# Kernel tuning notes

Hardware: AMD Instinct MI355X
Metric: run time of the kernel (lower is better)

Reference implementation:

```python
import jax, jax.numpy as jnp
import numpy as np

N = 1024   # nodes
E = 65536  # edges per relation
H = 2      # attention heads
NEG_SLOPE = 0.2


def _add_self_loops(ei, n):
    loop = jnp.arange(n, dtype=ei.dtype)
    return jnp.concatenate([ei, jnp.stack([loop, loop])], axis=1)


def _gat(x, ei, W, a_src, a_dst, bias, n):
    # PyG GATConv (heads=H, concat=True): project, edge attention, segment softmax, scatter-sum
    h, c = a_src.shape
    xp = (x @ W).reshape(n, h, c)                      # [n, H, C]
    src, dst = ei[0], ei[1]
    al_s = jnp.einsum('nhc,hc->nh', xp, a_src)         # [n, H]
    al_d = jnp.einsum('nhc,hc->nh', xp, a_dst)
    alpha = jax.nn.leaky_relu(al_s[src] + al_d[dst], NEG_SLOPE)  # [E, H]
    m = jax.ops.segment_max(alpha, dst, num_segments=n)
    m = jnp.where(jnp.isfinite(m), m, 0.0)
    m = jax.lax.stop_gradient(m)
    e = jnp.exp(alpha - m[dst])
    s = jax.ops.segment_sum(e, dst, num_segments=n)
    a = e / (s[dst] + 1e-16)                           # segment softmax over incoming edges
    out = jax.ops.segment_sum(xp[src] * a[:, :, None], dst, num_segments=n)
    return out.reshape(n, h * c) + bias


def setup_inputs():
    key = jax.random.key(0)
    ks = jax.random.split(key, 32)
    d = {}
    d['x'] = jax.random.normal(ks[0], (N, 256), dtype=jnp.float32)
    d['ei0'] = jax.random.randint(ks[1], (2, E), 0, N)
    d['ei1'] = jax.random.randint(ks[2], (2, E), 0, N)
    k = 3
    # layer 1: in 256 -> H*256 = 512 per relation
    for r in range(2):
        d[f'W1_{r}'] = jax.random.normal(ks[k], (256, H * 256), jnp.float32) * 0.0625; k += 1
        d[f'as1_{r}'] = jax.random.normal(ks[k], (H, 256), jnp.float32) * 0.0625; k += 1
        d[f'ad1_{r}'] = jax.random.normal(ks[k], (H, 256), jnp.float32) * 0.0625; k += 1
        d[f'b1_{r}'] = jnp.zeros((H * 256,), jnp.float32)
    # layer 2: in 512 -> H*64 = 128 per relation
    for r in range(2):
        d[f'W2_{r}'] = jax.random.normal(ks[k], (512, H * 64), jnp.float32) * 0.0442; k += 1
        d[f'as2_{r}'] = jax.random.normal(ks[k], (H, 64), jnp.float32) * 0.125; k += 1
        d[f'ad2_{r}'] = jax.random.normal(ks[k], (H, 64), jnp.float32) * 0.125; k += 1
        d[f'b2_{r}'] = jnp.zeros((H * 64,), jnp.float32)
    d['w_lin'] = jax.random.normal(ks[k], (H * 64, 1), jnp.float32) * 0.088; k += 1
    d['b_lin'] = jnp.zeros((1,), jnp.float32)
    return d


def reference(x, ei0, ei1, W1_0, as1_0, ad1_0, b1_0, W1_1, as1_1, ad1_1, b1_1,
              W2_0, as2_0, ad2_0, b2_0, W2_1, as2_1, ad2_1, b2_1, w_lin, b_lin):
    e0 = _add_self_loops(ei0, N)
    e1 = _add_self_loops(ei1, N)
    # HeteroConv aggr='sum' over the two relations
    h1 = _gat(x, e0, W1_0, as1_0, ad1_0, b1_0, N) + _gat(x, e1, W1_1, as1_1, ad1_1, b1_1, N)
    h1 = jax.nn.relu(h1)
    h2 = _gat(h1, e0, W2_0, as2_0, ad2_0, b2_0, N) + _gat(h1, e1, W2_1, as2_1, ad2_1, b2_1, N)
    # dense pairwise sum over all node pairs: [N*N, 128]
    pairs = (h2[:, None, :] + h2[None, :, :]).reshape(N * N, h2.shape[-1])
    return pairs @ w_lin + b_lin
```

## Files before the change

kernel.cpp:

```cpp
#include <hip/hip_runtime.h>
#include <hip/hip_bf16.h>


#define NEG_SLOPE 0.2f
static __device__ __forceinline__ float lrelu(float x){ return x > 0.f ? x : NEG_SLOPE * x; }

#define NN 1024
#define SLOTS 192

static __device__ __forceinline__ int norm_cnt(int raw){
    return raw < -1000000000 ? raw - (int)0xAAAAAAAAu : raw;
}

struct P {
    const float *x; const int *ei0, *ei1;
    const float *W1_0,*as1_0,*ad1_0,*b1_0, *W1_1,*as1_1,*ad1_1,*b1_1;
    const float *W2_0,*as2_0,*ad2_0,*b2_0, *W2_1,*as2_1,*ad2_1,*b2_1;
    const float *wlin, *blin;
    float *out;
    __hip_bfloat162 *xp1_0,*xp1_1;
    float *L1;
    float *wc;
    float *nb;
    float *q, *qb;
    int *cnt;
    unsigned short *eb;
    int E;
};

__global__ __launch_bounds__(256)
void k1_scatter_gemm1(P p){
    __shared__ float As[32][68];
    __shared__ float Bs[32][68];
    const int b = blockIdx.x, t = threadIdx.x;

    if (b < 128){
        const int TOT = p.E + NN;
        for (int i = b*256 + t; i < 2*TOT; i += 128*256){
            int r = i >= TOT, e = i - r*TOT;
            const int* ei = r ? p.ei1 : p.ei0;
            int src, dst;
            if (e < p.E){ src = ei[e]; dst = ei[p.E + e]; } else { src = dst = e - p.E; }
            int pos = norm_cnt(atomicAdd(&p.cnt[r*NN + dst], 1));
            if (pos >= 0 && pos < SLOTS)
                p.eb[(dst*2 + r)*SLOTS + pos] = (unsigned short)src;
        }
        return;
    }
    if (b >= 384){
        int idx2 = b - 384;
        int r = idx2 >> 2, k0 = (idx2 & 3) * 128;
        const float* W2 = r ? p.W2_1 : p.W2_0;
        const float* as2 = r ? p.as2_1 : p.as2_0;
        const float* ad2 = r ? p.ad2_1 : p.ad2_0;
        if (t < 128){
            int k = k0 + t;
            float sa[2] = {0.f,0.f}, da[2] = {0.f,0.f}, za[2] = {0.f,0.f};
            #pragma unroll
            for (int h = 0; h < 2; h++){
                for (int c = 0; c < 64; c++){
                    float w = W2[k*128 + h*64 + c];
                    sa[h] += w * as2[h*64 + c];
                    da[h] += w * ad2[h*64 + c];
                    za[h] += w * p.wlin[h*64 + c];
                }
            }
            float* wcr = p.wc + r*6*512;
            wcr[0*512 + k] = sa[0]; wcr[1*512 + k] = sa[1];
            wcr[2*512 + k] = da[0]; wcr[3*512 + k] = da[1];
            wcr[4*512 + k] = za[0]; wcr[5*512 + k] = za[1];
        }
        if (b == 384 && t == 128){
            float s = 0.f;
            for (int k = 0; k < 128; k++) s += (p.b2_0[k] + p.b2_1[k]) * p.wlin[k];
            p.qb[0] = s;
        }
        return;
    }
    int idx = b - 128;
    int r = idx >> 7, t2 = idx & 127;
    int m0 = (t2 >> 3) * 64, n0 = (t2 & 7) * 64;
    const float* B = r ? p.W1_1 : p.W1_0;
    __hip_bfloat162* C = r ? p.xp1_1 : p.xp1_0;
    int tx = t & 15, ty = t >> 4;
    const int am0 = t >> 3,  ac40 = t & 7;
    const int am1 = (256+t) >> 3, ac41 = t & 7;
    const int bk0 = t >> 4,  bc40 = t & 15;
    const int bk1 = (256+t) >> 4, bc41 = t & 15;
    float acc[4][4] = {};
    float4 a4[2], b4[2];
    a4[0] = *(const float4*)(p.x + (size_t)(m0+am0)*256 + 0 + ac40*4);
    a4[1] = *(const float4*)(p.x + (size_t)(m0+am1)*256 + 0 + ac41*4);
    b4[0] = *(const float4*)(B + (size_t)(0+bk0)*512 + n0 + bc40*4);
    b4[1] = *(const float4*)(B + (size_t)(0+bk1)*512 + n0 + bc41*4);
    for (int k0 = 0; k0 < 256; k0 += 32){
        __syncthreads();
        As[ac40*4+0][am0] = a4[0].x; As[ac40*4+1][am0] = a4[0].y;
        As[ac40*4+2][am0] = a4[0].z; As[ac40*4+3][am0] = a4[0].w;
        As[ac41*4+0][am1] = a4[1].x; As[ac41*4+1][am1] = a4[1].y;
        As[ac41*4+2][am1] = a4[1].z; As[ac41*4+3][am1] = a4[1].w;
        *(float4*)&Bs[bk0][bc40*4] = b4[0];
        *(float4*)&Bs[bk1][bc41*4] = b4[1];
        __syncthreads();
        if (k0 + 32 < 256){
            int kn = k0 + 32;
            a4[0] = *(const float4*)(p.x + (size_t)(m0+am0)*256 + kn + ac40*4);
            a4[1] = *(const float4*)(p.x + (size_t)(m0+am1)*256 + kn + ac41*4);
            b4[0] = *(const float4*)(B + (size_t)(kn+bk0)*512 + n0 + bc40*4);
            b4[1] = *(const float4*)(B + (size_t)(kn+bk1)*512 + n0 + bc41*4);
        }
        #pragma unroll
        for (int kk = 0; kk < 32; kk++){
            float4 av = *(const float4*)&As[kk][ty*4];
            float4 bv = *(const float4*)&Bs[kk][tx*4];
            float ar[4] = {av.x, av.y, av.z, av.w};
            float br[4] = {bv.x, bv.y, bv.z, bv.w};
            #pragma unroll
            for (int i = 0; i < 4; i++)
                #pragma unroll
                for (int j = 0; j < 4; j++)
                    acc[i][j] += ar[i] * br[j];
        }
    }
    #pragma unroll
    for (int i = 0; i < 4; i++){
        int row = m0 + ty*4 + i, col = n0 + tx*4;
        __hip_bfloat162 t0, t1;
        t0.x = __float2bfloat16(acc[i][0]); t0.y = __float2bfloat16(acc[i][1]);
        t1.x = __float2bfloat16(acc[i][2]); t1.y = __float2bfloat16(acc[i][3]);
        size_t o2 = ((size_t)row*512 + col) >> 1;
        C[o2] = t0; C[o2 + 1] = t1;
    }
    {
        int h = n0 >> 8;
        const float* as_ = r ? p.as1_1 : p.as1_0;
        const float* ad_ = r ? p.ad1_1 : p.ad1_0;
        float a_s[4], a_d[4];
        #pragma unroll
        for (int u = 0; u < 4; u++){
            a_s[u] = as_[n0 + tx*4 + u];
            a_d[u] = ad_[n0 + tx*4 + u];
        }
        #pragma unroll
        for (int i = 0; i < 4; i++){
            float ps = acc[i][0]*a_s[0] + acc[i][1]*a_s[1]
                     + acc[i][2]*a_s[2] + acc[i][3]*a_s[3];
            float pd = acc[i][0]*a_d[0] + acc[i][1]*a_d[1]
                     + acc[i][2]*a_d[2] + acc[i][3]*a_d[3];
            #pragma unroll
            for (int o = 8; o > 0; o >>= 1){
                ps += __shfl_down(ps, o, 16);
                pd += __shfl_down(pd, o, 16);
            }
            if (tx == 0){
                int row = m0 + ty*4 + i;
                atomicAdd(&p.L1[row*8 + r*4 + h],     ps);
                atomicAdd(&p.L1[row*8 + r*4 + 2 + h], pd);
            }
        }
    }
}

__global__ __launch_bounds__(256)
void k2_agg1(P p){
    __shared__ float wa0[256], wa1[256];
    __shared__ int ssrc[256];
    __shared__ float rr0[4], rr1[4], invs[2];
    __shared__ float pacc[4][64][8];
    const int v = blockIdx.x, t = threadIdx.x;
    const int par = t >> 6;
    const int c16 = t & 63;
    const bool head0 = c16 < 32;
    float acc[8] = {};
    #pragma unroll
    for (int r = 0; r < 2; r++){
        const __hip_bfloat162* xp = r ? p.xp1_1 : p.xp1_0;
        const unsigned short* eb = p.eb + (v*2 + r)*SLOTS;
        int end = min(norm_cnt(p.cnt[r*NN + v]), SLOTS);
        float ad0 = p.L1[v*8 + r*4 + 2], ad1 = p.L1[v*8 + r*4 + 3];
        float s0 = 0.f, s1 = 0.f;
        if (t < end){
            int s = eb[t];
            s0 = __expf(lrelu(p.L1[s*8 + r*4 + 0] + ad0));
            s1 = __expf(lrelu(p.L1[s*8 + r*4 + 1] + ad1));
            ssrc[t] = s * 256;
            wa0[t] = s0;
            wa1[t] = s1;
        }
        #pragma unroll
        for (int o = 32; o > 0; o >>= 1){
            s0 += __shfl_down(s0, o, 64);
            s1 += __shfl_down(s1, o, 64);
        }
        if ((t & 63) == 0){ rr0[t>>6] = s0; rr1[t>>6] = s1; }
        __syncthreads();
        if (t == 0){
            float S0 = 0.f, S1 = 0.f;
            #pragma unroll
            for (int i = 0; i < 4; i++){ S0 += rr0[i]; S1 += rr1[i]; }
            invs[0] = 1.f / (S0 + 1e-16f);
            invs[1] = 1.f / (S1 + 1e-16f);
        }
        __syncthreads();
        const float inv = head0 ? invs[0] : invs[1];
        #pragma unroll 4
        for (int i = par; i < end; i += 4){
            const __hip_bfloat162* rp = xp + ssrc[i] + c16*4;
            float4 raw = *(const float4*)rp;
            const __hip_bfloat162* w = (const __hip_bfloat162*)&raw;
            float a = (head0 ? wa0[i] : wa1[i]) * inv;
            #pragma unroll
            for (int u = 0; u < 4; u++){
                acc[2*u+0] += __bfloat162float(w[u].x) * a;
                acc[2*u+1] += __bfloat162float(w[u].y) * a;
            }
        }
        __syncthreads();
    }
    #pragma unroll
    for (int u = 0; u < 8; u++) pacc[par][c16][u] = acc[u];
    __syncthreads();
    if (par == 0){
        int cb = c16 * 8;
        float o[8];
        #pragma unroll
        for (int u = 0; u < 8; u++){
            float s = acc[u] + pacc[1][c16][u] + pacc[2][c16][u] + pacc[3][c16][u];
            s += p.b1_0[cb+u] + p.b1_1[cb+u];
            o[u] = s > 0.f ? s : 0.f;
        }
        const int slot[6] = {0, 1, 4, 5, 2, 3};
        #pragma unroll
        for (int r2 = 0; r2 < 2; r2++){
            #pragma unroll
            for (int j = 0; j < 6; j++){
                const float* w = p.wc + ((r2*6 + j) << 9) + cb;
                float s = o[0]*w[0] + o[1]*w[1] + o[2]*w[2] + o[3]*w[3]
                        + o[4]*w[4] + o[5]*w[5] + o[6]*w[6] + o[7]*w[7];
                #pragma unroll
                for (int off = 32; off > 0; off >>= 1) s += __shfl_down(s, off, 64);
                if (c16 == 0) p.nb[(v*2 + r2)*8 + slot[j]] = s;
            }
        }
    }
}

__global__ __launch_bounds__(256)
void k3_agg2(P p){
    __shared__ float red[2][2][4];
    const int b = blockIdx.x, t = threadIdx.x, lane = t & 63, wave = t >> 6;
    const int nl = wave >> 1, r = wave & 1;
    const int v = b*2 + nl;
    const unsigned short* eb = p.eb + (v*2 + r)*SLOTS;
    int end = min(norm_cnt(p.cnt[r*NN + v]), SLOTS);
    const float* nbv = p.nb + (v*2 + r)*8;
    float ld0 = nbv[4], ld1 = nbv[5];
    float d0 = 0.f, d1 = 0.f, n0 = 0.f, n1 = 0.f;
    for (int e = lane; e < end; e += 64){
        int s = eb[e];
        float4 g = *(const float4*)(p.nb + (s*2 + r)*8);
        float e0 = __expf(lrelu(g.x + ld0));
        float e1 = __expf(lrelu(g.y + ld1));
        d0 += e0; d1 += e1;
        n0 += e0 * g.z; n1 += e1 * g.w;
    }
    #pragma unroll
    for (int o = 1; o < 64; o <<= 1){
        d0 += __shfl_xor(d0, o, 64); d1 += __shfl_xor(d1, o, 64);
        n0 += __shfl_xor(n0, o, 64); n1 += __shfl_xor(n1, o, 64);
    }
    if (lane == 0){
        red[nl][r][0] = d0; red[nl][r][1] = d1;
        red[nl][r][2] = n0; red[nl][r][3] = n1;
    }
    __syncthreads();
    if (t == nl*128){
        float qv = p.qb[0];
        #pragma unroll
        for (int rr = 0; rr < 2; rr++){
            qv += red[nl][rr][2] / (red[nl][rr][0] + 1e-16f);
            qv += red[nl][rr][3] / (red[nl][rr][1] + 1e-16f);
        }
        p.q[v] = qv;
    }
}

__global__ __launch_bounds__(256)
void k4_pairs(P p){
    int i = blockIdx.x, t = threadIdx.x;
    float qi = p.q[i] + p.blin[0];
    float4 qj = ((const float4*)p.q)[t];
    float4 o = { qi + qj.x, qi + qj.y, qi + qj.z, qi + qj.w };
    ((float4*)p.out)[(size_t)i * 256 + t] = o;
}

extern "C" void kernel_launch(void* const* d_in, const int* in_sizes, int n_in,
                              void* d_out, int out_size, void* d_ws, size_t ws_size,
                              hipStream_t stream){
    P prm;
    prm.x    = (const float*)d_in[0];
    prm.ei0  = (const int*)d_in[1];
    prm.ei1  = (const int*)d_in[2];
    prm.W1_0 = (const float*)d_in[3];  prm.as1_0 = (const float*)d_in[4];
    prm.ad1_0 = (const float*)d_in[5]; prm.b1_0  = (const float*)d_in[6];
    prm.W1_1 = (const float*)d_in[7];  prm.as1_1 = (const float*)d_in[8];
    prm.ad1_1 = (const float*)d_in[9]; prm.b1_1  = (const float*)d_in[10];
    prm.W2_0 = (const float*)d_in[11]; prm.as2_0 = (const float*)d_in[12];
    prm.ad2_0 = (const float*)d_in[13]; prm.b2_0 = (const float*)d_in[14];
    prm.W2_1 = (const float*)d_in[15]; prm.as2_1 = (const float*)d_in[16];
    prm.ad2_1 = (const float*)d_in[17]; prm.b2_1 = (const float*)d_in[18];
    prm.wlin = (const float*)d_in[19];
    prm.blin = (const float*)d_in[20];
    prm.out  = (float*)d_out;
    prm.E    = in_sizes[1] / 2;
    const int N = NN;

    char* wp = (char*)d_ws;
    auto alloc = [&](size_t bytes) -> char* {
        char* r = wp; wp += (bytes + 255) & ~(size_t)255; return r;
    };
    prm.xp1_0 = (__hip_bfloat162*)alloc((size_t)N*512*2);
    prm.xp1_1 = (__hip_bfloat162*)alloc((size_t)N*512*2);
    prm.cnt = (int*)alloc((size_t)2*N*4);
    prm.L1  = (float*)alloc((size_t)N*8*4);
    prm.wc  = (float*)alloc((size_t)2*6*512*4);
    prm.nb  = (float*)alloc((size_t)N*2*8*4);
    prm.eb  = (unsigned short*)alloc((size_t)N*2*SLOTS*2);
    prm.q   = (float*)alloc(N*4);
    prm.qb  = (float*)alloc(256);

    k1_scatter_gemm1<<<392, 256, 0, stream>>>(prm);
    k2_agg1<<<NN, 256, 0, stream>>>(prm);
    k3_agg2<<<NN/2, 256, 0, stream>>>(prm);
    k4_pairs<<<NN, 256, 0, stream>>>(prm);
}
```

Baseline: 149.7 us.

## Merge per-relation softmax setup, spread layer-2 projections, batch pair rows

In k2_agg1, the attention weights and softmax denominators for both relations are computed in one pass up front, which removes two barriers per relation. The final projections are split across all four waves instead of only wave 0. In k1, the W2 collapse loop is vectorised with float4 loads, and k3 peels its first edge iteration so the loads start early. k4 now writes four output rows per block with a quarter of the blocks. The edge-index and L1 reads are speculative and can touch uninitialised slots, though those results are masked out.

Measured after the change: 145.9 us. 1.03x faster.

```diff
diff --git a/kernel.cpp b/kernel.cpp
--- a/kernel.cpp
+++ b/kernel.cpp
@@ -55,14 +55,19 @@
         const float* ad2 = r ? p.ad2_1 : p.ad2_0;
         if (t < 128){
             int k = k0 + t;
+            const float* row = W2 + k*128;
             float sa[2] = {0.f,0.f}, da[2] = {0.f,0.f}, za[2] = {0.f,0.f};
             #pragma unroll
             for (int h = 0; h < 2; h++){
-                for (int c = 0; c < 64; c++){
-                    float w = W2[k*128 + h*64 + c];
-                    sa[h] += w * as2[h*64 + c];
-                    da[h] += w * ad2[h*64 + c];
-                    za[h] += w * p.wlin[h*64 + c];
+                #pragma unroll
+                for (int c4 = 0; c4 < 16; c4++){
+                    float4 w  = *(const float4*)(row + h*64 + c4*4);
+                    float4 av = *(const float4*)(as2 + h*64 + c4*4);
+                    float4 dv = *(const float4*)(ad2 + h*64 + c4*4);
+                    float4 zv = *(const float4*)(p.wlin + h*64 + c4*4);
+                    sa[h] += w.x*av.x + w.y*av.y + w.z*av.z + w.w*av.w;
+                    da[h] += w.x*dv.x + w.y*dv.y + w.z*dv.z + w.w*dv.w;
+                    za[h] += w.x*zv.x + w.y*zv.y + w.z*zv.z + w.w*zv.w;
                 }
             }
             float* wcr = p.wc + r*6*512;
@@ -163,84 +168,100 @@
 
 __global__ __launch_bounds__(256)
 void k2_agg1(P p){
-    __shared__ float wa0[256], wa1[256];
-    __shared__ int ssrc[256];
-    __shared__ float rr0[4], rr1[4], invs[2];
+    __shared__ float wa0[2][SLOTS], wa1[2][SLOTS];
+    __shared__ int   ssrc[2][SLOTS];
+    __shared__ float rsum[4][2];
+    __shared__ float invs[2][2];
     __shared__ float pacc[4][64][8];
     const int v = blockIdx.x, t = threadIdx.x;
     const int par = t >> 6;
     const int c16 = t & 63;
     const bool head0 = c16 < 32;
+
+    const int r1 = t >> 7, slot1 = t & 127;
+    int endv[2];
+    endv[0] = min(norm_cnt(p.cnt[v]),      SLOTS);
+    endv[1] = min(norm_cnt(p.cnt[NN + v]), SLOTS);
+    int sA = p.eb[(v*2 + r1)*SLOTS + slot1];
+    const bool xact = (par == 0) || (par == 2);
+    const int r2x = (par == 2) ? 1 : 0;
+    const int slot2 = 128 + (t & 63);
+    int sB = p.eb[(v*2 + r2x)*SLOTS + slot2];
+    float2 ldv0 = *(const float2*)(p.L1 + v*8 + 0*4 + 2);
+    float2 ldv1 = *(const float2*)(p.L1 + v*8 + 1*4 + 2);
+    float2 ldA = r1  ? ldv1 : ldv0;
+    float2 ldB = r2x ? ldv1 : ldv0;
+    float2 lsA = *(const float2*)(p.L1 + sA*8 + r1*4);
+    float2 lsB = *(const float2*)(p.L1 + sB*8 + r2x*4);
+    bool actA = slot1 < endv[r1];
+    bool actB = xact && (slot2 < endv[r2x]);
+    float e0 = actA ? __expf(lrelu(lsA.x + ldA.x)) : 0.f;
+    float e1 = actA ? __expf(lrelu(lsA.y + ldA.y)) : 0.f;
+    float f0 = actB ? __expf(lrelu(lsB.x + ldB.x)) : 0.f;
+    float f1 = actB ? __expf(lrelu(lsB.y + ldB.y)) : 0.f;
+    if (actA){ wa0[r1][slot1] = e0; wa1[r1][slot1] = e1; ssrc[r1][slot1] = sA*256; }
+    if (actB){ wa0[r2x][slot2] = f0; wa1[r2x][slot2] = f1; ssrc[r2x][slot2] = sB*256; }
+    float s0 = e0 + f0, s1 = e1 + f1;
+    #pragma unroll
+    for (int o = 32; o > 0; o >>= 1){
+        s0 += __shfl_down(s0, o, 64);
+        s1 += __shfl_down(s1, o, 64);
+    }
+    if (c16 == 0){ rsum[par][0] = s0; rsum[par][1] = s1; }
+    __syncthreads();
+    if (t == 0){
+        invs[0][0] = 1.f / (rsum[0][0] + rsum[1][0] + 1e-16f);
+        invs[0][1] = 1.f / (rsum[0][1] + rsum[1][1] + 1e-16f);
+        invs[1][0] = 1.f / (rsum[2][0] + rsum[3][0] + 1e-16f);
+        invs[1][1] = 1.f / (rsum[2][1] + rsum[3][1] + 1e-16f);
+    }
+    __syncthreads();
+
     float acc[8] = {};
     #pragma unroll
     for (int r = 0; r < 2; r++){
         const __hip_bfloat162* xp = r ? p.xp1_1 : p.xp1_0;
-        const unsigned short* eb = p.eb + (v*2 + r)*SLOTS;
-        int end = min(norm_cnt(p.cnt[r*NN + v]), SLOTS);
-        float ad0 = p.L1[v*8 + r*4 + 2], ad1 = p.L1[v*8 + r*4 + 3];
-        float s0 = 0.f, s1 = 0.f;
-        if (t < end){
-            int s = eb[t];
-            s0 = __expf(lrelu(p.L1[s*8 + r*4 + 0] + ad0));
-            s1 = __expf(lrelu(p.L1[s*8 + r*4 + 1] + ad1));
-            ssrc[t] = s * 256;
-            wa0[t] = s0;
-            wa1[t] = s1;
-        }
-        #pragma unroll
-        for (int o = 32; o > 0; o >>= 1){
-            s0 += __shfl_down(s0, o, 64);
-            s1 += __shfl_down(s1, o, 64);
-        }
-        if ((t & 63) == 0){ rr0[t>>6] = s0; rr1[t>>6] = s1; }
-        __syncthreads();
-        if (t == 0){
-            float S0 = 0.f, S1 = 0.f;
-            #pragma unroll
-            for (int i = 0; i < 4; i++){ S0 += rr0[i]; S1 += rr1[i]; }
-            invs[0] = 1.f / (S0 + 1e-16f);
-            invs[1] = 1.f / (S1 + 1e-16f);
-        }
-        __syncthreads();
-        const float inv = head0 ? invs[0] : invs[1];
+        const int end = endv[r];
+        const float inv = head0 ? invs[r][0] : invs[r][1];
         #pragma unroll 4
         for (int i = par; i < end; i += 4){
-            const __hip_bfloat162* rp = xp + ssrc[i] + c16*4;
+            const __hip_bfloat162* rp = xp + ssrc[r][i] + c16*4;
             float4 raw = *(const float4*)rp;
             const __hip_bfloat162* w = (const __hip_bfloat162*)&raw;
-            float a = (head0 ? wa0[i] : wa1[i]) * inv;
+            float a = (head0 ? wa0[r][i] : wa1[r][i]) * inv;
             #pragma unroll
             for (int u = 0; u < 4; u++){
                 acc[2*u+0] += __bfloat162float(w[u].x) * a;
                 acc[2*u+1] += __bfloat162float(w[u].y) * a;
             }
         }
-        __syncthreads();
-    }
+    }
+    __syncthreads();
     #pragma unroll
     for (int u = 0; u < 8; u++) pacc[par][c16][u] = acc[u];
     __syncthreads();
-    if (par == 0){
+
+    {
         int cb = c16 * 8;
         float o[8];
         #pragma unroll
         for (int u = 0; u < 8; u++){
-            float s = acc[u] + pacc[1][c16][u] + pacc[2][c16][u] + pacc[3][c16][u];
+            float s = pacc[0][c16][u] + pacc[1][c16][u]
+                    + pacc[2][c16][u] + pacc[3][c16][u];
             s += p.b1_0[cb+u] + p.b1_1[cb+u];
             o[u] = s > 0.f ? s : 0.f;
         }
         const int slot[6] = {0, 1, 4, 5, 2, 3};
         #pragma unroll
-        for (int r2 = 0; r2 < 2; r2++){
-            #pragma unroll
-            for (int j = 0; j < 6; j++){
-                const float* w = p.wc + ((r2*6 + j) << 9) + cb;
-                float s = o[0]*w[0] + o[1]*w[1] + o[2]*w[2] + o[3]*w[3]
-                        + o[4]*w[4] + o[5]*w[5] + o[6]*w[6] + o[7]*w[7];
-                #pragma unroll
-                for (int off = 32; off > 0; off >>= 1) s += __shfl_down(s, off, 64);
-                if (c16 == 0) p.nb[(v*2 + r2)*8 + slot[j]] = s;
-            }
+        for (int k = 0; k < 3; k++){
+            int idx = par*3 + k;
+            int r2 = idx / 6, j = idx % 6;
+            const float* w = p.wc + ((r2*6 + j) << 9) + cb;
+            float s = o[0]*w[0] + o[1]*w[1] + o[2]*w[2] + o[3]*w[3]
+                    + o[4]*w[4] + o[5]*w[5] + o[6]*w[6] + o[7]*w[7];
+            #pragma unroll
+            for (int off = 32; off > 0; off >>= 1) s += __shfl_down(s, off, 64);
+            if (c16 == 0) p.nb[(v*2 + r2)*8 + slot[j]] = s;
         }
     }
 }
@@ -252,17 +273,24 @@
     const int nl = wave >> 1, r = wave & 1;
     const int v = b*2 + nl;
     const unsigned short* eb = p.eb + (v*2 + r)*SLOTS;
+    int s_pre = eb[lane];
     int end = min(norm_cnt(p.cnt[r*NN + v]), SLOTS);
     const float* nbv = p.nb + (v*2 + r)*8;
     float ld0 = nbv[4], ld1 = nbv[5];
-    float d0 = 0.f, d1 = 0.f, n0 = 0.f, n1 = 0.f;
-    for (int e = lane; e < end; e += 64){
+    float4 g0 = *(const float4*)(p.nb + (s_pre*2 + r)*8);
+    bool act = lane < end;
+    float e0 = act ? __expf(lrelu(g0.x + ld0)) : 0.f;
+    float e1 = act ? __expf(lrelu(g0.y + ld1)) : 0.f;
+    float d0 = e0, d1 = e1;
+    float n0 = act ? e0 * g0.z : 0.f;
+    float n1 = act ? e1 * g0.w : 0.f;
+    for (int e = lane + 64; e < end; e += 64){
         int s = eb[e];
         float4 g = *(const float4*)(p.nb + (s*2 + r)*8);
-        float e0 = __expf(lrelu(g.x + ld0));
-        float e1 = __expf(lrelu(g.y + ld1));
-        d0 += e0; d1 += e1;
-        n0 += e0 * g.z; n1 += e1 * g.w;
+        float a0 = __expf(lrelu(g.x + ld0));
+        float a1 = __expf(lrelu(g.y + ld1));
+        d0 += a0; d1 += a1;
+        n0 += a0 * g.z; n1 += a1 * g.w;
     }
     #pragma unroll
     for (int o = 1; o < 64; o <<= 1){
@@ -287,11 +315,16 @@
 
 __global__ __launch_bounds__(256)
 void k4_pairs(P p){
-    int i = blockIdx.x, t = threadIdx.x;
-    float qi = p.q[i] + p.blin[0];
+    const int b = blockIdx.x, t = threadIdx.x;
     float4 qj = ((const float4*)p.q)[t];
-    float4 o = { qi + qj.x, qi + qj.y, qi + qj.z, qi + qj.w };
-    ((float4*)p.out)[(size_t)i * 256 + t] = o;
+    float bl = p.blin[0];
+    #pragma unroll
+    for (int ii = 0; ii < 4; ++ii){
+        int i = b*4 + ii;
+        float qi = p.q[i] + bl;
+        float4 o = { qi + qj.x, qi + qj.y, qi + qj.z, qi + qj.w };
+        ((float4*)p.out)[(size_t)i * 256 + t] = o;
+    }
 }
 
 extern "C" void kernel_launch(void* const* d_in, const int* in_sizes, int n_in,
@@ -332,5 +365,5 @@
     k1_scatter_gemm1<<<392, 256, 0, stream>>>(prm);
     k2_agg1<<<NN, 256, 0, stream>>>(prm);
     k3_agg2<<<NN/2, 256, 0, stream>>>(prm);
-    k4_pairs<<<NN, 256, 0, stream>>>(prm);
-}
+    k4_pairs<<<NN/4, 256, 0, stream>>>(prm);
+}
```
